# Optimization experiments

Measured on AMD Instinct MI355X. Metric: run time of the kernel, lower is better.

Reference implementation:

```python
import jax, jax.numpy as jnp
import numpy as np
import math

TAU = 0.07
KD_T = 3.0
MOM = 0.5
POS_K = 1
NEG_K = 8192


def _kldiv(y_s, y_t, T):
    # F.kl_div(log_softmax(y_s/T), softmax(y_t/T), 'batchmean') * T^2
    log_ps = jax.nn.log_softmax(y_s / T, axis=1)
    log_pt = jax.nn.log_softmax(y_t / T, axis=1)
    pt = jnp.exp(log_pt)
    return jnp.sum(pt * (log_pt - log_ps)) / y_s.shape[0] * (T * T)


def setup_inputs() -> dict:
    key = jax.random.key(0)
    ks = jax.random.split(key, 6)
    B, D, N = 128, 128, 100000
    stdv = 1.0 / math.sqrt(D / 3)
    emb0 = jax.random.normal(ks[0], (B, D), dtype=jnp.float32)
    emb0 = emb0 / jnp.linalg.norm(emb0, axis=1, keepdims=True)
    emb1 = jax.random.normal(ks[1], (B, D), dtype=jnp.float32)
    emb1 = emb1 / jnp.linalg.norm(emb1, axis=1, keepdims=True)
    mem0 = jax.random.uniform(ks[2], (N, D), minval=-stdv, maxval=stdv, dtype=jnp.float32)
    mem1 = jax.random.uniform(ks[3], (N, D), minval=-stdv, maxval=stdv, dtype=jnp.float32)
    pos_idx = jax.random.randint(ks[4], (B, POS_K + 1), 0, N)
    neg_idx = jax.random.randint(ks[5], (B, NEG_K), 0, N)
    return {"emb0": emb0, "emb1": emb1, "mem0": mem0, "mem1": mem1,
            "pos_idx": pos_idx, "neg_idx": neg_idx}


def _simi(mem, emb, idx):
    # gather [B,K,D] rows from memory bank (detached) and dot with emb [B,D]
    rep = jax.lax.stop_gradient(mem[idx])
    return jnp.einsum('bkd,bd->bk', rep, emb) / TAU


def reference(emb0, emb1, mem0, mem1, pos_idx, neg_idx):
    embs = [emb0, emb1]
    mems = [mem0, mem1]
    n_net = 2
    idx = jnp.concatenate([pos_idx, neg_idx], axis=1)  # [B, 1+pos_k+neg_k]

    # ---- inter (cross-network) logits + soft ICL loss ----
    inter_logits = []
    soft_icl = jnp.float32(0.0)
    for i in range(n_net):
        for j in range(i + 1, n_net):
            cij = _simi(mems[i], embs[j], idx)
            cji = _simi(mems[j], embs[i], idx)
            inter_logits += [cij, cji]
            soft_icl = soft_icl + _kldiv(cij, jax.lax.stop_gradient(cji), KD_T)
            soft_icl = soft_icl + _kldiv(cji, jax.lax.stop_gradient(cij), KD_T)

    npos = POS_K + 1
    icl = jnp.float32(0.0)
    for logit in inter_logits:
        lp = logit - jax.nn.logsumexp(logit, axis=1, keepdims=True)
        icl = icl + (-jnp.mean(jnp.sum(lp[:, :npos], axis=1) / npos))

    # ---- intra (within-network) logits ----
    idx2 = idx[:, 1:]  # drop the first positive
    intra_logits = [_simi(mems[i], embs[i], idx2) for i in range(n_net)]

    soft_vcl = jnp.float32(0.0)
    for i in range(n_net):
        for j in range(n_net):
            if i != j:
                soft_vcl = soft_vcl + _kldiv(intra_logits[i], jax.lax.stop_gradient(intra_logits[j]), KD_T)

    vcl = jnp.float32(0.0)
    for logit in intra_logits:
        lp = logit - jax.nn.logsumexp(logit, axis=1, keepdims=True)
        vcl = vcl + (-jnp.mean(jnp.sum(lp[:, :POS_K], axis=1) / POS_K))

    # ---- momentum update + L2 normalize + scatter back (no grad) ----
    p0 = pos_idx[:, 0]
    new_mems = []
    for i in range(n_net):
        pos = mems[i][p0]
        upd = MOM * pos + (1.0 - MOM) * embs[i]
        upd = upd / jnp.sqrt(jnp.sum(upd * upd, axis=1, keepdims=True))
        new_mems.append(jax.lax.stop_gradient(mems[i].at[p0].set(upd)))

    return (vcl, soft_vcl, icl, soft_icl, new_mems[0], new_mems[1])
```

## Files before the change

kernel.cpp:

```cpp
#include <hip/hip_runtime.h>
#include <math.h>

#define B 128
#define D 128
#define NMEM 100000
#define KTOT 8194
#define NEGK 8192
#define CHUNKS 16
#define CS 513
#define N4 (NMEM * D / 4)

typedef float nt4 __attribute__((ext_vector_type(4)));

__global__ __launch_bounds__(256, 4) void gather_logits(
        const float* __restrict__ emb0, const float* __restrict__ emb1,
        const float* __restrict__ mem0, const float* __restrict__ mem1,
        const int* __restrict__ pos_idx, const int* __restrict__ neg_idx,
        float* __restrict__ partials) {
    const int c = blockIdx.x;
    const int b = blockIdx.y;
    const int tid = threadIdx.x;
    const int lane = tid & 63;
    const int w = tid >> 6;
    const int g = lane >> 3;
    const int l8 = lane & 7;
    const float INV_TAU = 1.0f / 0.07f;
    const float INV3 = 1.0f / 3.0f;

    float4 q0[4], q1[4];
    #pragma unroll
    for (int j = 0; j < 4; ++j) {
        q0[j] = *(const float4*)(emb0 + b * D + j * 32 + l8 * 4);
        q1[j] = *(const float4*)(emb1 + b * D + j * 32 + l8 * 4);
    }

    float s1ij = 0.f, s1ji = 0.f, s1i0 = 0.f, s1i1 = 0.f;
    float s3ij = 0.f, s3ji = 0.f, s3i0 = 0.f, s3i1 = 0.f;
    float wa = 0.f, wb = 0.f, wc = 0.f, wd = 0.f;

    __shared__ float red[4][12];
    __shared__ float sps[6];

    const int k0 = c * CS;
    const int kend = (k0 + CS < KTOT) ? k0 + CS : KTOT;
    const int kbase = k0 + w * 8 + g;
    const int posbase = b * 2;
    const int negbase = b * NEGK - 2;

    if (tid < 6) sps[tid] = 0.f;

    float4 A0[4], A1[4], B0[4], B1[4];

#define FETCH(IT, R0, R1) do {                                               \
    const int kf = kbase + (IT) * 32;                                        \
    const int kc = (kf < kend) ? kf : (kend - 1);                            \
    const int r = (kc < 2) ? pos_idx[posbase + kc] : neg_idx[negbase + kc];  \
    const float* p0 = mem0 + r * D + l8 * 4;                                 \
    const float* p1 = mem1 + r * D + l8 * 4;                                 \
    _Pragma("unroll")                                                        \
    for (int j = 0; j < 4; ++j) {                                            \
        R0[j] = *(const float4*)(p0 + j * 32);                               \
        R1[j] = *(const float4*)(p1 + j * 32);                               \
    }                                                                        \
} while (0)

#define COMPUTE(IT, R0, R1) do {                                             \
    const int kk = kbase + (IT) * 32;                                        \
    float pij = 0.f, pii = 0.f, pji = 0.f, pjj = 0.f;                        \
    _Pragma("unroll")                                                        \
    for (int j = 0; j < 4; ++j) {                                            \
        pij += R0[j].x * q1[j].x + R0[j].y * q1[j].y                         \
             + R0[j].z * q1[j].z + R0[j].w * q1[j].w;                        \
        pii += R0[j].x * q0[j].x + R0[j].y * q0[j].y                         \
             + R0[j].z * q0[j].z + R0[j].w * q0[j].w;                        \
        pji += R1[j].x * q0[j].x + R1[j].y * q0[j].y                         \
             + R1[j].z * q0[j].z + R1[j].w * q0[j].w;                        \
        pjj += R1[j].x * q1[j].x + R1[j].y * q1[j].y                         \
             + R1[j].z * q1[j].z + R1[j].w * q1[j].w;                        \
    }                                                                        \
    _Pragma("unroll")                                                        \
    for (int off = 1; off < 8; off <<= 1) {                                  \
        pij += __shfl_xor(pij, off, 64);                                     \
        pii += __shfl_xor(pii, off, 64);                                     \
        pji += __shfl_xor(pji, off, 64);                                     \
        pjj += __shfl_xor(pjj, off, 64);                                     \
    }                                                                        \
    const float mA = (kk < kend) ? 1.f : 0.f;                                \
    const float mI = (kk >= 1) ? mA : 0.f;                                   \
    const float cij = pij * INV_TAU, ci0 = pii * INV_TAU;                    \
    const float cji = pji * INV_TAU, ci1 = pjj * INV_TAU;                    \
    const float e3ij = __expf(cij * INV3), e3ji = __expf(cji * INV3);        \
    const float e3i0 = __expf(ci0 * INV3), e3i1 = __expf(ci1 * INV3);        \
    s1ij += mA * __expf(cij);                                                \
    s1ji += mA * __expf(cji);                                                \
    s3ij += mA * e3ij;                                                       \
    s3ji += mA * e3ji;                                                       \
    wa += mA * e3ji * (cji - cij);                                           \
    wb += mA * e3ij * (cij - cji);                                           \
    s1i0 += mI * __expf(ci0);                                                \
    s1i1 += mI * __expf(ci1);                                                \
    s3i0 += mI * e3i0;                                                       \
    s3i1 += mI * e3i1;                                                       \
    wc += mI * e3i1 * (ci1 - ci0);                                           \
    wd += mI * e3i0 * (ci0 - ci1);                                           \
    if (kk == 0 && l8 == 0) { sps[0] = cij; sps[2] = cji; }                  \
    if (kk == 1 && l8 == 0) { sps[1] = cij; sps[3] = cji;                    \
                              sps[4] = ci0; sps[5] = ci1; }                  \
} while (0)

    FETCH(0, A0, A1);
    for (int it = 0; it < 16; it += 2) {
        FETCH(it + 1, B0, B1);
        COMPUTE(it, A0, A1);
        FETCH(it + 2, A0, A1);
        COMPUTE(it + 1, B0, B1);
    }
    COMPUTE(16, A0, A1);

#undef FETCH
#undef COMPUTE

    float v[12] = {s1ij, s1ji, s1i0, s1i1, s3ij, s3ji, s3i0, s3i1, wa, wb, wc, wd};
    #pragma unroll
    for (int j = 0; j < 12; ++j) {
        v[j] += __shfl_xor(v[j], 8, 64);
        v[j] += __shfl_xor(v[j], 16, 64);
        v[j] += __shfl_xor(v[j], 32, 64);
    }
    if (lane == 0) {
        #pragma unroll
        for (int j = 0; j < 12; ++j) red[w][j] = v[j];
    }
    __syncthreads();
    float* outp = partials + (b * CHUNKS + c) * 20;
    if (tid < 12) outp[tid] = red[0][tid] + red[1][tid] + red[2][tid] + red[3][tid];
    else if (tid < 18) outp[tid] = sps[tid - 12];
}

__global__ void copy_mems(const nt4* __restrict__ m0, const nt4* __restrict__ m1,
                          nt4* __restrict__ o0, nt4* __restrict__ o1) {
    for (int i = blockIdx.x * blockDim.x + threadIdx.x; i < N4; i += gridDim.x * blockDim.x) {
        nt4 a = m0[i];
        nt4 b = m1[i];
        __builtin_nontemporal_store(a, o0 + i);
        __builtin_nontemporal_store(b, o1 + i);
    }
}

__global__ void final_update(const float* __restrict__ partials, float* __restrict__ out,
                             const float* __restrict__ emb0, const float* __restrict__ emb1,
                             const float* __restrict__ mem0, const float* __restrict__ mem1,
                             const int* __restrict__ pos_idx,
                             float* __restrict__ o0, float* __restrict__ o1) {
    if (blockIdx.x < B) {
        const int b = blockIdx.x;
        const int tid = threadIdx.x;
        const int lane = tid & 63;
        const int net = tid >> 6;
        const int p0 = pos_idx[b * 2];
        bool skip = false;
        for (int b2 = b + 1; b2 < B; ++b2)
            if (pos_idx[b2 * 2] == p0) skip = true;
        if (skip) return;
        const float* mem = net ? mem1 : mem0;
        const float* emb = net ? emb1 : emb0;
        float* o = net ? o1 : o0;
        const float2 mv = *(const float2*)(mem + p0 * D + 2 * lane);
        const float2 ev = *(const float2*)(emb + b * D + 2 * lane);
        const float ux = 0.5f * mv.x + 0.5f * ev.x;
        const float uy = 0.5f * mv.y + 0.5f * ev.y;
        float ss = ux * ux + uy * uy;
        #pragma unroll
        for (int off = 1; off < 64; off <<= 1) ss += __shfl_xor(ss, off, 64);
        const float inv = 1.0f / sqrtf(ss);
        float2 wv; wv.x = ux * inv; wv.y = uy * inv;
        *(float2*)(o + p0 * D + 2 * lane) = wv;
        return;
    }
    const int b = threadIdx.x;
    float a[12];
    #pragma unroll
    for (int j = 0; j < 12; ++j) a[j] = 0.f;
    for (int c = 0; c < CHUNKS; ++c) {
        const float* p = partials + (b * CHUNKS + c) * 20;
        #pragma unroll
        for (int j = 0; j < 12; ++j) a[j] += p[j];
    }
    const float* e = partials + (b * CHUNKS) * 20 + 12;
    const float cij0 = e[0], cij1 = e[1], cji0 = e[2], cji1 = e[3], i01 = e[4], i11 = e[5];
    const float icl_b = -((cij0 + cij1) * 0.5f - __logf(a[0]))
                        - ((cji0 + cji1) * 0.5f - __logf(a[1]));
    const float vcl_b = -(i01 - __logf(a[2])) - (i11 - __logf(a[3]));
    const float sicl_b = 3.0f * (a[8] / a[5] + a[9] / a[4]);
    const float svcl_b = 3.0f * (a[10] / a[7] + a[11] / a[6]);
    __shared__ float r[4][128];
    r[0][b] = vcl_b; r[1][b] = svcl_b; r[2][b] = icl_b; r[3][b] = sicl_b;
    __syncthreads();
    for (int s = 64; s > 0; s >>= 1) {
        if (b < s) {
            r[0][b] += r[0][b + s]; r[1][b] += r[1][b + s];
            r[2][b] += r[2][b + s]; r[3][b] += r[3][b + s];
        }
        __syncthreads();
    }
    if (b == 0) {
        out[0] = r[0][0] * (1.0f / 128.f);
        out[1] = r[1][0] * (1.0f / 128.f);
        out[2] = r[2][0] * (1.0f / 128.f);
        out[3] = r[3][0] * (1.0f / 128.f);
    }
}

extern "C" void kernel_launch(void* const* d_in, const int* in_sizes, int n_in,
                              void* d_out, int out_size, void* d_ws, size_t ws_size,
                              hipStream_t stream) {
    const float* emb0 = (const float*)d_in[0];
    const float* emb1 = (const float*)d_in[1];
    const float* mem0 = (const float*)d_in[2];
    const float* mem1 = (const float*)d_in[3];
    const int* pos_idx = (const int*)d_in[4];
    const int* neg_idx = (const int*)d_in[5];
    float* out = (float*)d_out;
    float* partials = (float*)d_ws;

    float* out_m0 = out + 4;
    float* out_m1 = out + 4 + NMEM * D;

    gather_logits<<<dim3(CHUNKS, B), 256, 0, stream>>>(emb0, emb1, mem0, mem1,
                                                       pos_idx, neg_idx, partials);
    copy_mems<<<4096, 256, 0, stream>>>((const nt4*)mem0, (const nt4*)mem1,
                                        (nt4*)out_m0, (nt4*)out_m1);
    final_update<<<B + 1, 128, 0, stream>>>(partials, out, emb0, emb1,
                                            mem0, mem1, pos_idx, out_m0, out_m1);
}
```

Baseline: 331.7 us.

## Invert gather into per-memory-row bucketed traversal via counting sort

Builds a histogram, prefix scan and scatter of all (b,k) indices bucketed by memory row, then processes each memory row once, loading mem0/mem1 rows a single time and computing the needed dot products for every reference to that row. Per-batch softmax and KL accumulators are combined with LDS atomics and then global atomics. This replaces random row gathers with a streaming pass over both memory banks, at the cost of extra kernels (a single-block scan over 100k entries), many atomics and nondeterministic float summation order. The old path is kept as a fallback when the workspace is too small.

```diff
diff --git a/kernel.cpp b/kernel.cpp
--- a/kernel.cpp
+++ b/kernel.cpp
@@ -6,11 +6,227 @@
 #define NMEM 100000
 #define KTOT 8194
 #define NEGK 8192
+#define NREF (B * KTOT)
 #define CHUNKS 16
 #define CS 513
 #define N4 (NMEM * D / 4)
 
+#define ROWS_PER_BLK 64
+#define NBLK_MAIN ((NMEM + ROWS_PER_BLK - 1) / ROWS_PER_BLK)
+
+#define WS_CNT 0u
+#define WS_START 400000u
+#define WS_ENTRIES 800016u
+#define WS_PARTIALS 4995344u
+#define WS_SP 5001488u
+#define WS_NEED 5004560u
+
 typedef float nt4 __attribute__((ext_vector_type(4)));
+
+
+__global__ void zero_k(unsigned* __restrict__ cnt, float* __restrict__ partials_g,
+                       float* __restrict__ sp_g) {
+    const int i = blockIdx.x * 256 + threadIdx.x;
+    if (i < NMEM) cnt[i] = 0u;
+    if (i < 128 * 12) partials_g[i] = 0.f;
+    if (i < 128 * 6) sp_g[i] = 0.f;
+}
+
+__global__ void hist_k(const int* __restrict__ pos_idx, const int* __restrict__ neg_idx,
+                       unsigned* __restrict__ cnt) {
+    const int b = blockIdx.y;
+    const int k = blockIdx.x * 256 + threadIdx.x;
+    if (k >= KTOT) return;
+    const int r = (k < 2) ? pos_idx[b * 2 + k] : neg_idx[b * NEGK + k - 2];
+    atomicAdd(&cnt[r], 1u);
+}
+
+#define SCAN_PER 98
+__global__ __launch_bounds__(1024) void scan_k(const unsigned* __restrict__ cnt,
+                                               unsigned* __restrict__ start,
+                                               unsigned* __restrict__ ofs) {
+    __shared__ unsigned lds[1024];
+    const int t = threadIdx.x;
+    const int base = t * SCAN_PER;
+    unsigned sum = 0;
+    for (int i = 0; i < SCAN_PER; ++i) {
+        const int idx = base + i;
+        if (idx < NMEM) sum += cnt[idx];
+    }
+    lds[t] = sum;
+    __syncthreads();
+    for (int off = 1; off < 1024; off <<= 1) {
+        const unsigned v = (t >= off) ? lds[t - off] : 0u;
+        __syncthreads();
+        lds[t] += v;
+        __syncthreads();
+    }
+    unsigned run = (t == 0) ? 0u : lds[t - 1];
+    for (int i = 0; i < SCAN_PER; ++i) {
+        const int idx = base + i;
+        if (idx < NMEM) {
+            start[idx] = run;
+            ofs[idx] = run;
+            run += cnt[idx];
+        }
+    }
+    if (t == 0) start[NMEM] = NREF;
+}
+
+__global__ void scatter_k(const int* __restrict__ pos_idx, const int* __restrict__ neg_idx,
+                          unsigned* __restrict__ ofs, unsigned* __restrict__ entries) {
+    const int b = blockIdx.y;
+    const int k = blockIdx.x * 256 + threadIdx.x;
+    if (k >= KTOT) return;
+    const int r = (k < 2) ? pos_idx[b * 2 + k] : neg_idx[b * NEGK + k - 2];
+    const unsigned p = atomicAdd(&ofs[r], 1u);
+    entries[p] = ((unsigned)b << 14) | (unsigned)k;
+}
+
+__global__ __launch_bounds__(256) void main_gather(
+        const float* __restrict__ emb0, const float* __restrict__ emb1,
+        const float* __restrict__ mem0, const float* __restrict__ mem1,
+        const unsigned* __restrict__ start, const unsigned* __restrict__ entries,
+        float* __restrict__ partials_g, float* __restrict__ sp_g) {
+    const int tid = threadIdx.x;
+    const int lane = tid & 63;
+    const int w = tid >> 6;
+    const int g = lane >> 3;
+    const int l8 = lane & 7;
+    const float INV_TAU = 1.0f / 0.07f;
+    const float INV3 = 1.0f / 3.0f;
+
+    __shared__ float accum[128][12];
+    for (int i = tid; i < 128 * 12; i += 256) ((float*)accum)[i] = 0.f;
+    __syncthreads();
+
+    const int n0 = blockIdx.x * ROWS_PER_BLK;
+    for (int rr = w; rr < ROWS_PER_BLK; rr += 4) {
+        const int n = n0 + rr;
+        if (n >= NMEM) break;
+        const unsigned s0 = start[n], s1 = start[n + 1];
+        if (s0 == s1) continue;
+        float4 r0[4], r1[4];
+        #pragma unroll
+        for (int j = 0; j < 4; ++j) {
+            r0[j] = *(const float4*)(mem0 + n * D + j * 32 + l8 * 4);
+            r1[j] = *(const float4*)(mem1 + n * D + j * 32 + l8 * 4);
+        }
+        for (unsigned e = s0; e < s1; e += 8) {
+            const unsigned ei = e + g;
+            const bool act = (ei < s1);
+            const unsigned ent = entries[act ? ei : (s1 - 1)];
+            const int b = (int)(ent >> 14);
+            const int k = (int)(ent & 0x3FFFu);
+            float pij = 0.f, pii = 0.f, pji = 0.f, pjj = 0.f;
+            #pragma unroll
+            for (int j = 0; j < 4; ++j) {
+                const float4 q0 = *(const float4*)(emb0 + b * D + j * 32 + l8 * 4);
+                const float4 q1 = *(const float4*)(emb1 + b * D + j * 32 + l8 * 4);
+                pij += r0[j].x * q1.x + r0[j].y * q1.y + r0[j].z * q1.z + r0[j].w * q1.w;
+                pii += r0[j].x * q0.x + r0[j].y * q0.y + r0[j].z * q0.z + r0[j].w * q0.w;
+                pji += r1[j].x * q0.x + r1[j].y * q0.y + r1[j].z * q0.z + r1[j].w * q0.w;
+                pjj += r1[j].x * q1.x + r1[j].y * q1.y + r1[j].z * q1.z + r1[j].w * q1.w;
+            }
+            #pragma unroll
+            for (int off = 1; off < 8; off <<= 1) {
+                pij += __shfl_xor(pij, off, 64);
+                pii += __shfl_xor(pii, off, 64);
+                pji += __shfl_xor(pji, off, 64);
+                pjj += __shfl_xor(pjj, off, 64);
+            }
+            if (act && l8 == 0) {
+                const float cij = pij * INV_TAU, ci0 = pii * INV_TAU;
+                const float cji = pji * INV_TAU, ci1 = pjj * INV_TAU;
+                const float e3ij = __expf(cij * INV3), e3ji = __expf(cji * INV3);
+                atomicAdd(&accum[b][0], __expf(cij));
+                atomicAdd(&accum[b][1], __expf(cji));
+                atomicAdd(&accum[b][4], e3ij);
+                atomicAdd(&accum[b][5], e3ji);
+                atomicAdd(&accum[b][8], e3ji * (cji - cij));
+                atomicAdd(&accum[b][9], e3ij * (cij - cji));
+                if (k >= 1) {
+                    const float e3i0 = __expf(ci0 * INV3), e3i1 = __expf(ci1 * INV3);
+                    atomicAdd(&accum[b][2], __expf(ci0));
+                    atomicAdd(&accum[b][3], __expf(ci1));
+                    atomicAdd(&accum[b][6], e3i0);
+                    atomicAdd(&accum[b][7], e3i1);
+                    atomicAdd(&accum[b][10], e3i1 * (ci1 - ci0));
+                    atomicAdd(&accum[b][11], e3i0 * (ci0 - ci1));
+                }
+                if (k == 0) { sp_g[b * 6 + 0] = cij; sp_g[b * 6 + 2] = cji; }
+                else if (k == 1) { sp_g[b * 6 + 1] = cij; sp_g[b * 6 + 3] = cji;
+                                   sp_g[b * 6 + 4] = ci0; sp_g[b * 6 + 5] = ci1; }
+            }
+        }
+    }
+    __syncthreads();
+    for (int i = tid; i < 128 * 12; i += 256) {
+        const float v = ((float*)accum)[i];
+        if (v != 0.f) atomicAdd(&partials_g[i], v);
+    }
+}
+
+__global__ void final2(const float* __restrict__ partials_g, const float* __restrict__ sp_g,
+                       float* __restrict__ out,
+                       const float* __restrict__ emb0, const float* __restrict__ emb1,
+                       const float* __restrict__ mem0, const float* __restrict__ mem1,
+                       const int* __restrict__ pos_idx,
+                       float* __restrict__ o0, float* __restrict__ o1) {
+    if (blockIdx.x < B) {
+        const int b = blockIdx.x;
+        const int tid = threadIdx.x;
+        const int lane = tid & 63;
+        const int net = tid >> 6;
+        const int p0 = pos_idx[b * 2];
+        bool skip = false;
+        for (int b2 = b + 1; b2 < B; ++b2)
+            if (pos_idx[b2 * 2] == p0) skip = true;
+        if (skip) return;
+        const float* mem = net ? mem1 : mem0;
+        const float* emb = net ? emb1 : emb0;
+        float* o = net ? o1 : o0;
+        const float2 mv = *(const float2*)(mem + p0 * D + 2 * lane);
+        const float2 ev = *(const float2*)(emb + b * D + 2 * lane);
+        const float ux = 0.5f * mv.x + 0.5f * ev.x;
+        const float uy = 0.5f * mv.y + 0.5f * ev.y;
+        float ss = ux * ux + uy * uy;
+        #pragma unroll
+        for (int off = 1; off < 64; off <<= 1) ss += __shfl_xor(ss, off, 64);
+        const float inv = 1.0f / sqrtf(ss);
+        float2 wv; wv.x = ux * inv; wv.y = uy * inv;
+        *(float2*)(o + p0 * D + 2 * lane) = wv;
+        return;
+    }
+    const int b = threadIdx.x;
+    float a[12];
+    #pragma unroll
+    for (int j = 0; j < 12; ++j) a[j] = partials_g[b * 12 + j];
+    const float* e = sp_g + b * 6;
+    const float cij0 = e[0], cij1 = e[1], cji0 = e[2], cji1 = e[3], i01 = e[4], i11 = e[5];
+    const float icl_b = -((cij0 + cij1) * 0.5f - __logf(a[0]))
+                        - ((cji0 + cji1) * 0.5f - __logf(a[1]));
+    const float vcl_b = -(i01 - __logf(a[2])) - (i11 - __logf(a[3]));
+    const float sicl_b = 3.0f * (a[8] / a[5] + a[9] / a[4]);
+    const float svcl_b = 3.0f * (a[10] / a[7] + a[11] / a[6]);
+    __shared__ float r[4][128];
+    r[0][b] = vcl_b; r[1][b] = svcl_b; r[2][b] = icl_b; r[3][b] = sicl_b;
+    __syncthreads();
+    for (int s = 64; s > 0; s >>= 1) {
+        if (b < s) {
+            r[0][b] += r[0][b + s]; r[1][b] += r[1][b + s];
+            r[2][b] += r[2][b + s]; r[3][b] += r[3][b + s];
+        }
+        __syncthreads();
+    }
+    if (b == 0) {
+        out[0] = r[0][0] * (1.0f / 128.f);
+        out[1] = r[1][0] * (1.0f / 128.f);
+        out[2] = r[2][0] * (1.0f / 128.f);
+        out[3] = r[3][0] * (1.0f / 128.f);
+    }
+}
+
 
 __global__ __launch_bounds__(256, 4) void gather_logits(
         const float* __restrict__ emb0, const float* __restrict__ emb1,
@@ -137,16 +353,6 @@
     else if (tid < 18) outp[tid] = sps[tid - 12];
 }
 
-__global__ void copy_mems(const nt4* __restrict__ m0, const nt4* __restrict__ m1,
-                          nt4* __restrict__ o0, nt4* __restrict__ o1) {
-    for (int i = blockIdx.x * blockDim.x + threadIdx.x; i < N4; i += gridDim.x * blockDim.x) {
-        nt4 a = m0[i];
-        nt4 b = m1[i];
-        __builtin_nontemporal_store(a, o0 + i);
-        __builtin_nontemporal_store(b, o1 + i);
-    }
-}
-
 __global__ void final_update(const float* __restrict__ partials, float* __restrict__ out,
                              const float* __restrict__ emb0, const float* __restrict__ emb1,
                              const float* __restrict__ mem0, const float* __restrict__ mem1,
@@ -211,6 +417,16 @@
     }
 }
 
+__global__ void copy_mems(const nt4* __restrict__ m0, const nt4* __restrict__ m1,
+                          nt4* __restrict__ o0, nt4* __restrict__ o1) {
+    for (int i = blockIdx.x * blockDim.x + threadIdx.x; i < N4; i += gridDim.x * blockDim.x) {
+        nt4 a = m0[i];
+        nt4 b = m1[i];
+        __builtin_nontemporal_store(a, o0 + i);
+        __builtin_nontemporal_store(b, o1 + i);
+    }
+}
+
 extern "C" void kernel_launch(void* const* d_in, const int* in_sizes, int n_in,
                               void* d_out, int out_size, void* d_ws, size_t ws_size,
                               hipStream_t stream) {
@@ -221,15 +437,35 @@
     const int* pos_idx = (const int*)d_in[4];
     const int* neg_idx = (const int*)d_in[5];
     float* out = (float*)d_out;
-    float* partials = (float*)d_ws;
-
     float* out_m0 = out + 4;
     float* out_m1 = out + 4 + NMEM * D;
-
-    gather_logits<<<dim3(CHUNKS, B), 256, 0, stream>>>(emb0, emb1, mem0, mem1,
-                                                       pos_idx, neg_idx, partials);
-    copy_mems<<<4096, 256, 0, stream>>>((const nt4*)mem0, (const nt4*)mem1,
-                                        (nt4*)out_m0, (nt4*)out_m1);
-    final_update<<<B + 1, 128, 0, stream>>>(partials, out, emb0, emb1,
-                                            mem0, mem1, pos_idx, out_m0, out_m1);
-}
+    char* ws = (char*)d_ws;
+
+    if (ws_size >= WS_NEED) {
+        unsigned* cnt = (unsigned*)(ws + WS_CNT);
+        unsigned* start = (unsigned*)(ws + WS_START);
+        unsigned* entries = (unsigned*)(ws + WS_ENTRIES);
+        float* partials_g = (float*)(ws + WS_PARTIALS);
+        float* sp_g = (float*)(ws + WS_SP);
+
+        zero_k<<<(NMEM + 255) / 256, 256, 0, stream>>>(cnt, partials_g, sp_g);
+        hist_k<<<dim3((KTOT + 255) / 256, B), 256, 0, stream>>>(pos_idx, neg_idx, cnt);
+        scan_k<<<1, 1024, 0, stream>>>(cnt, start, cnt);
+        scatter_k<<<dim3((KTOT + 255) / 256, B), 256, 0, stream>>>(pos_idx, neg_idx,
+                                                                   cnt, entries);
+        main_gather<<<NBLK_MAIN, 256, 0, stream>>>(emb0, emb1, mem0, mem1,
+                                                   start, entries, partials_g, sp_g);
+        copy_mems<<<4096, 256, 0, stream>>>((const nt4*)mem0, (const nt4*)mem1,
+                                            (nt4*)out_m0, (nt4*)out_m1);
+        final2<<<B + 1, 128, 0, stream>>>(partials_g, sp_g, out, emb0, emb1,
+                                          mem0, mem1, pos_idx, out_m0, out_m1);
+    } else {
+        float* partials = (float*)d_ws;
+        gather_logits<<<dim3(CHUNKS, B), 256, 0, stream>>>(emb0, emb1, mem0, mem1,
+                                                           pos_idx, neg_idx, partials);
+        copy_mems<<<4096, 256, 0, stream>>>((const nt4*)mem0, (const nt4*)mem1,
+                                            (nt4*)out_m0, (nt4*)out_m1);
+        final_update<<<B + 1, 128, 0, stream>>>(partials, out, emb0, emb1,
+                                                mem0, mem1, pos_idx, out_m0, out_m1);
+    }
+}
```

Measured after the change: 789.2 us. 138% more time.
